# Kernel tuning notes

Hardware: AMD Instinct MI355X
Metric: run time of the kernel (lower is better)

## Reference

```python
import jax, jax.numpy as jnp
import numpy as np

CD_WT = 5.0
CLASSIFY_WT = 1.0
B, N, M, NUM_CLASSES = 32, 2048, 2048, 6


def setup_inputs() -> dict:
    key = jax.random.key(0)
    k1, k2, k3, k4 = jax.random.split(key, 4)
    inst_shape = jax.random.normal(k1, (B, N, 3), dtype=jnp.float32)
    model = jax.random.normal(k2, (B, M, 3), dtype=jnp.float32)
    pred = jax.random.normal(k3, (B, NUM_CLASSES), dtype=jnp.float32)
    gt = jax.random.randint(k4, (B,), 0, NUM_CLASSES, dtype=jnp.int64)
    return {"inst_shape": inst_shape, "model": model, "pred": pred, "gt": gt}


def _chamfer(a, b):
    # a: [B,N,3], b: [B,M,3]; squared pairwise distances [B,N,M]
    # ||a-b||^2 = ||a||^2 + ||b||^2 - 2 a.b  (avoids [B,N,M,3] intermediate)
    a2 = jnp.sum(a * a, axis=-1)  # [B,N]
    b2 = jnp.sum(b * b, axis=-1)  # [B,M]
    ab = jnp.einsum('bnd,bmd->bnm', a, b)  # [B,N,M]
    d = a2[:, :, None] + b2[:, None, :] - 2.0 * ab  # [B,N,M]
    dist1 = jnp.min(d, axis=2)  # [B,N] nearest in b for each a
    dist2 = jnp.min(d, axis=1)  # [B,M] nearest in a for each b
    loss = jnp.mean(dist1) + jnp.mean(dist2)
    return loss, dist1, dist2


def _cross_entropy(logits, labels):
    # nn.CrossEntropyLoss with default mean reduction
    logp = jax.nn.log_softmax(logits, axis=-1)  # [B,C]
    nll = -jnp.take_along_axis(logp, labels[:, None], axis=-1)[:, 0]
    return jnp.mean(nll)


def reference(inst_shape, model, pred, gt):
    cd_loss, _, _ = _chamfer(inst_shape, model)
    classify_loss = _cross_entropy(pred, gt)
    total_loss = CD_WT * cd_loss + CLASSIFY_WT * classify_loss
    return (total_loss, cd_loss, classify_loss)
```

## Files before the change

kernel.cpp:

```cpp
#include <hip/hip_runtime.h>

typedef __attribute__((ext_vector_type(8)))  short short8;
typedef __attribute__((ext_vector_type(16))) float f32x16;
typedef __attribute__((ext_vector_type(16))) unsigned u32x16;

#define NPTS 2048
#define BATCH 32
#define NUM_CLASSES 6
#define THREADS 256
#define QT 2
#define CTILES 64

#define BF16_ONE ((short)0x3F80)
#define FMAX_BITS 0x7F7FFFFFu

__device__ __forceinline__ unsigned short f2bf(float x) {
    union { float f; unsigned u; } v; v.f = x;
    unsigned r = v.u + 0x7FFF + ((v.u >> 16) & 1);
    return (unsigned short)(r >> 16);
}
__device__ __forceinline__ float bf2f(unsigned short h) {
    union { unsigned u; float f; } v; v.u = ((unsigned)h) << 16; return v.f;
}
__device__ __forceinline__ unsigned f2u(float x) {
    union { float f; unsigned u; } v; v.f = x; return v.u;
}
__device__ __forceinline__ float u2f(unsigned x) {
    union { unsigned u; float f; } v; v.u = x; return v.f;
}
__device__ __forceinline__ unsigned umin2(unsigned a, unsigned b) {
    return a < b ? a : b;
}

__global__ __launch_bounds__(THREADS, 2) void chamfer_mfma32(
    const float* __restrict__ inst, const float* __restrict__ model,
    float* __restrict__ partial)
{
    __shared__ char  cands[NPTS * 32];
    __shared__ float wsum[4];

    const int blk   = blockIdx.x;
    const int dir   = blk >> 8;
    const int batch = (blk >> 3) & 31;
    const int qc    = blk & 7;
    const int tid   = threadIdx.x;
    const int lane  = tid & 63, wid = tid >> 6;
    const int lh    = lane >> 5, lr = lane & 31;

    const float* __restrict__ Q = dir ? model : inst;
    const float* __restrict__ C = dir ? inst  : model;

    const float* cb = C + (size_t)batch * NPTS * 3;
    for (int c = tid; c < NPTS; c += THREADS) {
        float bx = cb[c*3+0], by = cb[c*3+1], bz = cb[c*3+2];
        float m2x = -2.f*bx, m2y = -2.f*by, m2z = -2.f*bz;
        unsigned short hx = f2bf(m2x), hy = f2bf(m2y), hz = f2bf(m2z);
        unsigned short lx = f2bf(m2x - bf2f(hx));
        unsigned short ly = f2bf(m2y - bf2f(hy));
        unsigned short lz = f2bf(m2z - bf2f(hz));
        float b2 = fmaf(bx,bx, fmaf(by,by, bz*bz));
        unsigned short b2h = f2bf(b2);
        unsigned short b2l = f2bf(b2 - bf2f(b2h));
        short8 kg0 = { (short)hx,(short)hy,(short)hz,(short)hx,(short)hy,(short)hz,(short)lx,(short)ly };
        short8 kg1 = { (short)lz,(short)b2h,(short)b2l, BF16_ONE, BF16_ONE, 0,0,0 };
        char* tbase = cands + (c >> 5) * 1024 + (c & 31) * 16;
        *(short8*)(tbase)       = kg0;
        *(short8*)(tbase + 512) = kg1;
    }

    short8 af[QT];
    const float* qb = Q + ((size_t)batch * NPTS + (size_t)qc * 256) * 3;
    #pragma unroll
    for (int qt = 0; qt < QT; ++qt) {
        const int qi = (wid * QT + qt) * 32 + lr;
        float x = qb[qi*3+0], y = qb[qi*3+1], z = qb[qi*3+2];
        unsigned short hx = f2bf(x), hy = f2bf(y), hz = f2bf(z);
        unsigned short lx = f2bf(x - bf2f(hx));
        unsigned short ly = f2bf(y - bf2f(hy));
        unsigned short lz = f2bf(z - bf2f(hz));
        float a2 = fmaf(x,x, fmaf(y,y, z*z));
        unsigned short a2h = f2bf(a2);
        unsigned short a2l = f2bf(a2 - bf2f(a2h));
        if (lh == 0)
            af[qt] = (short8){ (short)hx,(short)hy,(short)hz,(short)lx,(short)ly,(short)lz,(short)hx,(short)hy };
        else
            af[qt] = (short8){ (short)hz, BF16_ONE, BF16_ONE, (short)a2h,(short)a2l, 0,0,0 };
    }
    __syncthreads();

    u32x16 mnU, mnU2;
    f32x16 zero16;
    #pragma unroll
    for (int r = 0; r < 16; ++r) { mnU[r] = FMAX_BITS; mnU2[r] = FMAX_BITS; zero16[r] = 0.f; }

    const char* cp = cands + lh * 512 + lr * 16;
    for (int ct = 0; ct < CTILES; ct += 2) {
        short8 b0 = *(const short8*)(cp);
        short8 b1 = *(const short8*)(cp + 1024);
        cp += 2048;
        {
            f32x16 a00 = __builtin_amdgcn_mfma_f32_32x32x16_bf16(af[0], b0, zero16, 0,0,0);
            f32x16 a01 = __builtin_amdgcn_mfma_f32_32x32x16_bf16(af[0], b1, zero16, 0,0,0);
            #pragma unroll
            for (int r = 0; r < 16; ++r)
                mnU[r] = umin2(umin2(f2u(a00[r]), f2u(a01[r])), mnU[r]);
        }
        {
            f32x16 a10 = __builtin_amdgcn_mfma_f32_32x32x16_bf16(af[1], b0, zero16, 0,0,0);
            f32x16 a11 = __builtin_amdgcn_mfma_f32_32x32x16_bf16(af[1], b1, zero16, 0,0,0);
            #pragma unroll
            for (int r = 0; r < 16; ++r)
                mnU2[r] = umin2(umin2(f2u(a10[r]), f2u(a11[r])), mnU2[r]);
        }
    }

    float s = 0.f;
    #pragma unroll
    for (int r = 0; r < 16; ++r) {
        unsigned v = mnU[r];
        v = umin2(v, (unsigned)__shfl_xor((int)v, 1, 64));
        v = umin2(v, (unsigned)__shfl_xor((int)v, 2, 64));
        v = umin2(v, (unsigned)__shfl_xor((int)v, 4, 64));
        v = umin2(v, (unsigned)__shfl_xor((int)v, 8, 64));
        v = umin2(v, (unsigned)__shfl_xor((int)v, 16, 64));
        s += u2f(v);
        unsigned w = mnU2[r];
        w = umin2(w, (unsigned)__shfl_xor((int)w, 1, 64));
        w = umin2(w, (unsigned)__shfl_xor((int)w, 2, 64));
        w = umin2(w, (unsigned)__shfl_xor((int)w, 4, 64));
        w = umin2(w, (unsigned)__shfl_xor((int)w, 8, 64));
        w = umin2(w, (unsigned)__shfl_xor((int)w, 16, 64));
        s += u2f(w);
    }
    s += __shfl_xor(s, 32, 64);
    if (lane == 0) wsum[wid] = s;
    __syncthreads();
    if (tid == 0) partial[blk] = (wsum[0] + wsum[1]) + (wsum[2] + wsum[3]);
}

__global__ __launch_bounds__(256) void finalize_kernel(
    const float* __restrict__ partial, const float* __restrict__ pred,
    const int* __restrict__ gt, float* __restrict__ out)
{
    __shared__ float s_ce[BATCH];
    __shared__ float wsum[4];
    const int tid = threadIdx.x;

    float v = partial[tid] + partial[tid + 256];
    #pragma unroll
    for (int o = 32; o > 0; o >>= 1) v += __shfl_down(v, o, 64);
    const int lane = tid & 63, wid = tid >> 6;
    if (lane == 0) wsum[wid] = v;

    if (tid < BATCH) {
        const float* row = pred + tid * NUM_CLASSES;
        float mx = row[0];
        #pragma unroll
        for (int c = 1; c < NUM_CLASSES; ++c) mx = fmaxf(mx, row[c]);
        float se = 0.f;
        #pragma unroll
        for (int c = 0; c < NUM_CLASSES; ++c) se += __expf(row[c] - mx);
        const int lbl = gt[tid];
        s_ce[tid] = -(row[lbl] - mx - __logf(se));
    }
    __syncthreads();

    if (tid == 0) {
        float cd_sum = (wsum[0] + wsum[1]) + (wsum[2] + wsum[3]);
        float cd = cd_sum / (float)(BATCH * NPTS);
        float ce = 0.f;
        for (int i = 0; i < BATCH; ++i) ce += s_ce[i];
        ce /= (float)BATCH;
        out[0] = 5.f * cd + ce;
        out[1] = cd;
        out[2] = ce;
    }
}

extern "C" void kernel_launch(void* const* d_in, const int* in_sizes, int n_in,
                              void* d_out, int out_size, void* d_ws, size_t ws_size,
                              hipStream_t stream) {
    const float* inst  = (const float*)d_in[0];
    const float* model = (const float*)d_in[1];
    const float* pred  = (const float*)d_in[2];
    const int*   gt    = (const int*)d_in[3];
    float* out     = (float*)d_out;
    float* partial = (float*)d_ws;

    chamfer_mfma32<<<512, THREADS, 0, stream>>>(inst, model, partial);
    finalize_kernel<<<1, 256, 0, stream>>>(partial, pred, gt, out);
}
```

Before: 19.60 us.

## Split candidate set across two blocks with separate min-combine kernel

Splits each query chunk's candidate set into two halves processed by separate blocks, doubling the grid to 1024 blocks and halving shared memory per block so occupancy can rise to 4 blocks per CU. Per-query minima are written to workspace and a new combine kernel takes the min across halves and sums them. This targets underutilization of the CUs with only 512 blocks, at the cost of an extra kernel launch and global round-trip of partial minima.

```diff
diff --git a/kernel.cpp b/kernel.cpp
--- a/kernel.cpp
+++ b/kernel.cpp
@@ -8,11 +8,14 @@
 #define BATCH 32
 #define NUM_CLASSES 6
 #define THREADS 256
-#define QT 2
-#define CTILES 64
-
+#define CC 2
+#define CANDS_BLK 1024
+#define CTILES 32
+#define QC 8
+#define GROUPS 512
 #define BF16_ONE ((short)0x3F80)
 #define FMAX_BITS 0x7F7FFFFFu
+#define PART_OFF (GROUPS * CC * 256)
 
 __device__ __forceinline__ unsigned short f2bf(float x) {
     union { float f; unsigned u; } v; v.f = x;
@@ -32,26 +35,29 @@
     return a < b ? a : b;
 }
 
-__global__ __launch_bounds__(THREADS, 2) void chamfer_mfma32(
+__global__ __launch_bounds__(THREADS, 4) void chamfer_pass1(
     const float* __restrict__ inst, const float* __restrict__ model,
-    float* __restrict__ partial)
+    float* __restrict__ pmin)
 {
-    __shared__ char  cands[NPTS * 32];
-    __shared__ float wsum[4];
+    __shared__ char cands[CANDS_BLK * 32];
 
     const int blk   = blockIdx.x;
-    const int dir   = blk >> 8;
-    const int batch = (blk >> 3) & 31;
-    const int qc    = blk & 7;
+    const int cc    = blk & 1;
+    const int qc    = (blk >> 1) & 7;
+    const int batch = (blk >> 4) & 31;
+    const int dir   = blk >> 9;
+    const int g     = (dir * BATCH + batch) * QC + qc;
     const int tid   = threadIdx.x;
     const int lane  = tid & 63, wid = tid >> 6;
     const int lh    = lane >> 5, lr = lane & 31;
 
-    const float* __restrict__ Q = dir ? model : inst;
-    const float* __restrict__ C = dir ? inst  : model;
-
-    const float* cb = C + (size_t)batch * NPTS * 3;
-    for (int c = tid; c < NPTS; c += THREADS) {
+    const float* __restrict__ Q  = dir ? model : inst;
+    const float* __restrict__ Cp = dir ? inst  : model;
+
+    const float* cb = Cp + ((size_t)batch * NPTS + (size_t)cc * CANDS_BLK) * 3;
+    #pragma unroll
+    for (int k = 0; k < CANDS_BLK / THREADS; ++k) {
+        const int c = tid + k * THREADS;
         float bx = cb[c*3+0], by = cb[c*3+1], bz = cb[c*3+2];
         float m2x = -2.f*bx, m2y = -2.f*by, m2z = -2.f*bz;
         unsigned short hx = f2bf(m2x), hy = f2bf(m2y), hz = f2bf(m2z);
@@ -68,11 +74,11 @@
         *(short8*)(tbase + 512) = kg1;
     }
 
-    short8 af[QT];
+    short8 af0, af1;
     const float* qb = Q + ((size_t)batch * NPTS + (size_t)qc * 256) * 3;
     #pragma unroll
-    for (int qt = 0; qt < QT; ++qt) {
-        const int qi = (wid * QT + qt) * 32 + lr;
+    for (int qt = 0; qt < 2; ++qt) {
+        const int qi = (wid * 2 + qt) * 32 + lr;
         float x = qb[qi*3+0], y = qb[qi*3+1], z = qb[qi*3+2];
         unsigned short hx = f2bf(x), hy = f2bf(y), hz = f2bf(z);
         unsigned short lx = f2bf(x - bf2f(hx));
@@ -81,10 +87,12 @@
         float a2 = fmaf(x,x, fmaf(y,y, z*z));
         unsigned short a2h = f2bf(a2);
         unsigned short a2l = f2bf(a2 - bf2f(a2h));
+        short8 f;
         if (lh == 0)
-            af[qt] = (short8){ (short)hx,(short)hy,(short)hz,(short)lx,(short)ly,(short)lz,(short)hx,(short)hy };
+            f = (short8){ (short)hx,(short)hy,(short)hz,(short)lx,(short)ly,(short)lz,(short)hx,(short)hy };
         else
-            af[qt] = (short8){ (short)hz, BF16_ONE, BF16_ONE, (short)a2h,(short)a2l, 0,0,0 };
+            f = (short8){ (short)hz, BF16_ONE, BF16_ONE, (short)a2h,(short)a2l, 0,0,0 };
+        if (qt == 0) af0 = f; else af1 = f;
     }
     __syncthreads();
 
@@ -99,43 +107,57 @@
         short8 b1 = *(const short8*)(cp + 1024);
         cp += 2048;
         {
-            f32x16 a00 = __builtin_amdgcn_mfma_f32_32x32x16_bf16(af[0], b0, zero16, 0,0,0);
-            f32x16 a01 = __builtin_amdgcn_mfma_f32_32x32x16_bf16(af[0], b1, zero16, 0,0,0);
+            f32x16 a00 = __builtin_amdgcn_mfma_f32_32x32x16_bf16(af0, b0, zero16, 0,0,0);
+            f32x16 a01 = __builtin_amdgcn_mfma_f32_32x32x16_bf16(af0, b1, zero16, 0,0,0);
             #pragma unroll
             for (int r = 0; r < 16; ++r)
                 mnU[r] = umin2(umin2(f2u(a00[r]), f2u(a01[r])), mnU[r]);
         }
         {
-            f32x16 a10 = __builtin_amdgcn_mfma_f32_32x32x16_bf16(af[1], b0, zero16, 0,0,0);
-            f32x16 a11 = __builtin_amdgcn_mfma_f32_32x32x16_bf16(af[1], b1, zero16, 0,0,0);
+            f32x16 a10 = __builtin_amdgcn_mfma_f32_32x32x16_bf16(af1, b0, zero16, 0,0,0);
+            f32x16 a11 = __builtin_amdgcn_mfma_f32_32x32x16_bf16(af1, b1, zero16, 0,0,0);
             #pragma unroll
             for (int r = 0; r < 16; ++r)
                 mnU2[r] = umin2(umin2(f2u(a10[r]), f2u(a11[r])), mnU2[r]);
         }
     }
 
-    float s = 0.f;
+    float* pb = pmin + ((size_t)g * CC + cc) * 256;
     #pragma unroll
     for (int r = 0; r < 16; ++r) {
+        const int crow = (r & 3) + 8 * (r >> 2) + 4 * lh;
         unsigned v = mnU[r];
         v = umin2(v, (unsigned)__shfl_xor((int)v, 1, 64));
         v = umin2(v, (unsigned)__shfl_xor((int)v, 2, 64));
         v = umin2(v, (unsigned)__shfl_xor((int)v, 4, 64));
         v = umin2(v, (unsigned)__shfl_xor((int)v, 8, 64));
         v = umin2(v, (unsigned)__shfl_xor((int)v, 16, 64));
-        s += u2f(v);
+        if (lr == 0) pb[(wid * 2 + 0) * 32 + crow] = u2f(v);
         unsigned w = mnU2[r];
         w = umin2(w, (unsigned)__shfl_xor((int)w, 1, 64));
         w = umin2(w, (unsigned)__shfl_xor((int)w, 2, 64));
         w = umin2(w, (unsigned)__shfl_xor((int)w, 4, 64));
         w = umin2(w, (unsigned)__shfl_xor((int)w, 8, 64));
         w = umin2(w, (unsigned)__shfl_xor((int)w, 16, 64));
-        s += u2f(w);
-    }
-    s += __shfl_xor(s, 32, 64);
+        if (lr == 0) pb[(wid * 2 + 1) * 32 + crow] = u2f(w);
+    }
+}
+
+__global__ __launch_bounds__(256) void combine_kernel(
+    const float* __restrict__ pmin, float* __restrict__ partial)
+{
+    const int g   = blockIdx.x;
+    const int tid = threadIdx.x;
+    const float* p0 = pmin + (size_t)g * CC * 256;
+    unsigned a = f2u(p0[tid]), b = f2u(p0[256 + tid]);
+    float s = u2f(umin2(a, b));
+    #pragma unroll
+    for (int o = 32; o > 0; o >>= 1) s += __shfl_down(s, o, 64);
+    __shared__ float wsum[4];
+    const int lane = tid & 63, wid = tid >> 6;
     if (lane == 0) wsum[wid] = s;
     __syncthreads();
-    if (tid == 0) partial[blk] = (wsum[0] + wsum[1]) + (wsum[2] + wsum[3]);
+    if (tid == 0) partial[g] = (wsum[0] + wsum[1]) + (wsum[2] + wsum[3]);
 }
 
 __global__ __launch_bounds__(256) void finalize_kernel(
@@ -166,8 +188,7 @@
     __syncthreads();
 
     if (tid == 0) {
-        float cd_sum = (wsum[0] + wsum[1]) + (wsum[2] + wsum[3]);
-        float cd = cd_sum / (float)(BATCH * NPTS);
+        float cd = ((wsum[0] + wsum[1]) + (wsum[2] + wsum[3])) / (float)(BATCH * NPTS);
         float ce = 0.f;
         for (int i = 0; i < BATCH; ++i) ce += s_ce[i];
         ce /= (float)BATCH;
@@ -184,9 +205,10 @@
     const float* model = (const float*)d_in[1];
     const float* pred  = (const float*)d_in[2];
     const int*   gt    = (const int*)d_in[3];
-    float* out     = (float*)d_out;
-    float* partial = (float*)d_ws;
-
-    chamfer_mfma32<<<512, THREADS, 0, stream>>>(inst, model, partial);
-    finalize_kernel<<<1, 256, 0, stream>>>(partial, pred, gt, out);
-}
+    float* out = (float*)d_out;
+    float* ws  = (float*)d_ws;
+
+    chamfer_pass1<<<GROUPS * CC, THREADS, 0, stream>>>(inst, model, ws);
+    combine_kernel<<<GROUPS, 256, 0, stream>>>(ws, ws + PART_OFF);
+    finalize_kernel<<<1, 256, 0, stream>>>(ws + PART_OFF, pred, gt, out);
+}
```

After: 24.41 us. 1.25x slower.

## Software-pipeline MFMA tiles so min-reduction overlaps next tile's matrix ops

Applied to the files above, without the earlier changes.

Restructures the candidate loop into a prologue/steady-state/epilogue pipeline. Each iteration issues the next tile's four MFMAs and prefetches the following LDS tile before reducing the previous tile's results, so VALU min work can overlap MFMA latency. This raises live accumulator registers (eight f32x16 in flight), which may increase VGPR/AGPR pressure under the two-blocks-per-CU launch bound.

```diff
diff --git a/kernel.cpp b/kernel.cpp
--- a/kernel.cpp
+++ b/kernel.cpp
@@ -8,9 +8,6 @@
 #define BATCH 32
 #define NUM_CLASSES 6
 #define THREADS 256
-#define QT 2
-#define CTILES 64
-
 #define BF16_ONE ((short)0x3F80)
 #define FMAX_BITS 0x7F7FFFFFu
 
@@ -68,11 +65,11 @@
         *(short8*)(tbase + 512) = kg1;
     }
 
-    short8 af[QT];
+    short8 af0, af1;
     const float* qb = Q + ((size_t)batch * NPTS + (size_t)qc * 256) * 3;
     #pragma unroll
-    for (int qt = 0; qt < QT; ++qt) {
-        const int qi = (wid * QT + qt) * 32 + lr;
+    for (int qt = 0; qt < 2; ++qt) {
+        const int qi = (wid * 2 + qt) * 32 + lr;
         float x = qb[qi*3+0], y = qb[qi*3+1], z = qb[qi*3+2];
         unsigned short hx = f2bf(x), hy = f2bf(y), hz = f2bf(z);
         unsigned short lx = f2bf(x - bf2f(hx));
@@ -81,10 +78,12 @@
         float a2 = fmaf(x,x, fmaf(y,y, z*z));
         unsigned short a2h = f2bf(a2);
         unsigned short a2l = f2bf(a2 - bf2f(a2h));
+        short8 f;
         if (lh == 0)
-            af[qt] = (short8){ (short)hx,(short)hy,(short)hz,(short)lx,(short)ly,(short)lz,(short)hx,(short)hy };
+            f = (short8){ (short)hx,(short)hy,(short)hz,(short)lx,(short)ly,(short)lz,(short)hx,(short)hy };
         else
-            af[qt] = (short8){ (short)hz, BF16_ONE, BF16_ONE, (short)a2h,(short)a2l, 0,0,0 };
+            f = (short8){ (short)hz, BF16_ONE, BF16_ONE, (short)a2h,(short)a2l, 0,0,0 };
+        if (qt == 0) af0 = f; else af1 = f;
     }
     __syncthreads();
 
@@ -94,23 +93,48 @@
     for (int r = 0; r < 16; ++r) { mnU[r] = FMAX_BITS; mnU2[r] = FMAX_BITS; zero16[r] = 0.f; }
 
     const char* cp = cands + lh * 512 + lr * 16;
-    for (int ct = 0; ct < CTILES; ct += 2) {
-        short8 b0 = *(const short8*)(cp);
-        short8 b1 = *(const short8*)(cp + 1024);
+    short8 c0 = *(const short8*)(cp);
+    short8 c1 = *(const short8*)(cp + 1024);
+    short8 n0 = *(const short8*)(cp + 2048);
+    short8 n1 = *(const short8*)(cp + 3072);
+    cp += 4096;
+    f32x16 p00 = __builtin_amdgcn_mfma_f32_32x32x16_bf16(af0, c0, zero16, 0,0,0);
+    f32x16 p01 = __builtin_amdgcn_mfma_f32_32x32x16_bf16(af0, c1, zero16, 0,0,0);
+    f32x16 p10 = __builtin_amdgcn_mfma_f32_32x32x16_bf16(af1, c0, zero16, 0,0,0);
+    f32x16 p11 = __builtin_amdgcn_mfma_f32_32x32x16_bf16(af1, c1, zero16, 0,0,0);
+
+    #pragma unroll 2
+    for (int s = 1; s < 31; ++s) {
+        c0 = n0; c1 = n1;
+        n0 = *(const short8*)(cp);
+        n1 = *(const short8*)(cp + 1024);
         cp += 2048;
-        {
-            f32x16 a00 = __builtin_amdgcn_mfma_f32_32x32x16_bf16(af[0], b0, zero16, 0,0,0);
-            f32x16 a01 = __builtin_amdgcn_mfma_f32_32x32x16_bf16(af[0], b1, zero16, 0,0,0);
-            #pragma unroll
-            for (int r = 0; r < 16; ++r)
-                mnU[r] = umin2(umin2(f2u(a00[r]), f2u(a01[r])), mnU[r]);
+        f32x16 q00 = __builtin_amdgcn_mfma_f32_32x32x16_bf16(af0, c0, zero16, 0,0,0);
+        f32x16 q01 = __builtin_amdgcn_mfma_f32_32x32x16_bf16(af0, c1, zero16, 0,0,0);
+        f32x16 q10 = __builtin_amdgcn_mfma_f32_32x32x16_bf16(af1, c0, zero16, 0,0,0);
+        f32x16 q11 = __builtin_amdgcn_mfma_f32_32x32x16_bf16(af1, c1, zero16, 0,0,0);
+        #pragma unroll
+        for (int r = 0; r < 16; ++r)
+            mnU[r]  = umin2(umin2(f2u(p00[r]), f2u(p01[r])), mnU[r]);
+        #pragma unroll
+        for (int r = 0; r < 16; ++r)
+            mnU2[r] = umin2(umin2(f2u(p10[r]), f2u(p11[r])), mnU2[r]);
+        p00 = q00; p01 = q01; p10 = q10; p11 = q11;
+    }
+    {
+        f32x16 q00 = __builtin_amdgcn_mfma_f32_32x32x16_bf16(af0, n0, zero16, 0,0,0);
+        f32x16 q01 = __builtin_amdgcn_mfma_f32_32x32x16_bf16(af0, n1, zero16, 0,0,0);
+        f32x16 q10 = __builtin_amdgcn_mfma_f32_32x32x16_bf16(af1, n0, zero16, 0,0,0);
+        f32x16 q11 = __builtin_amdgcn_mfma_f32_32x32x16_bf16(af1, n1, zero16, 0,0,0);
+        #pragma unroll
+        for (int r = 0; r < 16; ++r) {
+            mnU[r]  = umin2(umin2(f2u(p00[r]), f2u(p01[r])), mnU[r]);
+            mnU2[r] = umin2(umin2(f2u(p10[r]), f2u(p11[r])), mnU2[r]);
         }
-        {
-            f32x16 a10 = __builtin_amdgcn_mfma_f32_32x32x16_bf16(af[1], b0, zero16, 0,0,0);
-            f32x16 a11 = __builtin_amdgcn_mfma_f32_32x32x16_bf16(af[1], b1, zero16, 0,0,0);
-            #pragma unroll
-            for (int r = 0; r < 16; ++r)
-                mnU2[r] = umin2(umin2(f2u(a10[r]), f2u(a11[r])), mnU2[r]);
+        #pragma unroll
+        for (int r = 0; r < 16; ++r) {
+            mnU[r]  = umin2(umin2(f2u(q00[r]), f2u(q01[r])), mnU[r]);
+            mnU2[r] = umin2(umin2(f2u(q10[r]), f2u(q11[r])), mnU2[r]);
         }
     }
 
```

Measured after the change: 18.95 us. 1.03x faster.
